# Performance work log

Hardware: AMD Instinct MI355X
Metric: run time of the kernel (lower is better)

Reference implementation:

```python
import jax, jax.numpy as jnp
import numpy as np

N_NODES = 50000
N_EDGES = 800000
HIDDEN = 128
NUM_GDL = 2


def setup_inputs() -> dict:
    key = jax.random.key(0)
    k0, k1, k2, k3, k4 = jax.random.split(key, 5)
    x = jax.random.normal(k0, (N_NODES, HIDDEN), dtype=jnp.float32)
    row = jax.random.randint(k1, (N_EDGES,), 0, N_NODES, dtype=jnp.int32)
    # ensure every node appears at least once as a target so degree >= 1
    col_tail = jax.random.randint(k2, (N_EDGES - N_NODES,), 0, N_NODES, dtype=jnp.int32)
    col = jnp.concatenate([jnp.arange(N_NODES, dtype=jnp.int32), col_tail])
    edge_index = jnp.stack([row, col], axis=0)  # [2, E]
    W1s = jax.random.normal(k3, (NUM_GDL, HIDDEN, HIDDEN), dtype=jnp.float32) / np.sqrt(HIDDEN).astype(np.float32)
    W2s = jax.random.normal(k4, (NUM_GDL, HIDDEN, 2 * HIDDEN), dtype=jnp.float32) / np.sqrt(2 * HIDDEN).astype(np.float32)
    biases = jnp.zeros((NUM_GDL, HIDDEN), dtype=jnp.float32)  # reset_parameters zeroes bias
    return {"x": x, "edge_index": edge_index, "W1s": W1s, "W2s": W2s, "biases": biases}


def reference(x, edge_index, W1s, W2s, biases):
    # eval mode: dropout is identity
    row, col = edge_index[0], edge_index[1]  # row = source j, col = target i
    n, d = x.shape
    deg = jax.ops.segment_sum(jnp.ones(row.shape[0], x.dtype), col, num_segments=n)
    norm = (1.0 / deg)[row]  # per-edge norm, indexed by row as in torch source
    for k in range(W1s.shape[0]):
        W1, W2, b = W1s[k], W2s[k], biases[k]
        # lin2(cat[x_i, x_j]) = x_i @ W2[:, :d].T + x_j @ W2[:, d:].T
        # precompute both node-level projections, then gather per edge (cheaper than per-edge GEMM)
        proj_i = x @ W2[:, :d].T  # [n, d]
        proj_j = x @ W2[:, d:].T  # [n, d]
        msg = norm[:, None] * (proj_i[col] + proj_j[row])  # [E, d]
        agg = jax.ops.segment_sum(msg, col, num_segments=n)  # scatter-add into targets
        out = x @ W1.T - agg + b
        x = jax.nn.gelu(out, approximate=False)  # torch nn.GELU default = exact erf
    return x
```

## Files before the change

kernel.cpp:

```cpp
#include <hip/hip_runtime.h>

#define N_NODES 50000
#define N_EDGES 800000
#define D 128
#define NBUCKET 196
#define CAP 8192
#define EPT 16
#define SCAT_BLOCKS 196
#define WCONV_BLOCKS 96
#define GEMM_TILES 782

typedef unsigned short ushort_t;
typedef __bf16 bf16x8 __attribute__((ext_vector_type(8)));
typedef float f32x4 __attribute__((ext_vector_type(4)));
typedef float f32x2 __attribute__((ext_vector_type(2)));

__device__ __forceinline__ ushort_t f2bf(float f) {
    unsigned u = __builtin_bit_cast(unsigned, f);
    u += 0x7FFFu + ((u >> 16) & 1u);
    return (ushort_t)(u >> 16);
}
__device__ __forceinline__ float bf2f(unsigned h16) {
    return __builtin_bit_cast(float, h16 << 16);
}
__device__ __forceinline__ bf16x8 pack8(float4 p0, float4 p1) {
    ushort_t __attribute__((aligned(16))) t[8] =
        { f2bf(p0.x), f2bf(p0.y), f2bf(p0.z), f2bf(p0.w),
          f2bf(p1.x), f2bf(p1.y), f2bf(p1.z), f2bf(p1.w) };
    return __builtin_bit_cast(bf16x8, *(const uint4*)t);
}

__global__ __launch_bounds__(256) void k_pre(const int* __restrict__ row, const int* __restrict__ col,
                                             int* __restrict__ bucket_cursor, unsigned* __restrict__ temp,
                                             const float* __restrict__ W1s, const float* __restrict__ W2s,
                                             ushort_t* __restrict__ Wb) {
    __shared__ int hist[NBUCKET];
    int b = blockIdx.x;
    if (b < SCAT_BLOCKS) {
        for (int t = threadIdx.x; t < NBUCKET; t += 256) hist[t] = 0;
        __syncthreads();
        int base = (b * 256 + threadIdx.x) * EPT;
        bool act = base < N_EDGES;
        int4 c[4], r[4];
        if (act) {
            #pragma unroll
            for (int q = 0; q < 4; ++q) c[q] = *(const int4*)(col + base + q * 4);
            #pragma unroll
            for (int q = 0; q < 4; ++q) r[q] = *(const int4*)(row + base + q * 4);
            #pragma unroll
            for (int q = 0; q < 4; ++q) {
                atomicAdd(&hist[c[q].x >> 8], 1); atomicAdd(&hist[c[q].y >> 8], 1);
                atomicAdd(&hist[c[q].z >> 8], 1); atomicAdd(&hist[c[q].w >> 8], 1);
            }
        }
        __syncthreads();
        for (int t = threadIdx.x; t < NBUCKET; t += 256) {
            int cnt = hist[t];
            hist[t] = cnt ? atomicAdd(&bucket_cursor[t], cnt) : 0;
        }
        __syncthreads();
        if (act) {
            #pragma unroll
            for (int q = 0; q < 4; ++q) {
                int cc[4] = { c[q].x, c[q].y, c[q].z, c[q].w };
                int rr[4] = { r[q].x, r[q].y, r[q].z, r[q].w };
                #pragma unroll
                for (int e = 0; e < 4; ++e) {
                    int bk = cc[e] >> 8;
                    int pos = atomicAdd(&hist[bk], 1);
                    temp[bk * CAP + pos] = (unsigned)rr[e] | ((unsigned)(cc[e] & 255) << 16);
                }
            }
        }
    } else {
        int c = (b - SCAT_BLOCKS) * 256 + threadIdx.x;
        int k = c / 12288, rem = c % 12288;
        int mat = rem / 4096, rr = (rem % 4096) / 32, col4 = rem % 32;
        const float* src = (mat == 0)
            ? (W1s + k * 16384 + rr * 128 + col4 * 4)
            : (W2s + k * 32768 + rr * 256 + (mat == 2 ? 128 : 0) + col4 * 4);
        float4 v = *(const float4*)src;
        ushort_t tmp[4] = { f2bf(v.x), f2bf(v.y), f2bf(v.z), f2bf(v.w) };
        *(uint2*)(Wb + ((size_t)(k * 3 + mat)) * 16384 + rr * 128 + col4 * 4) = *(const uint2*)tmp;
    }
}

template<bool AF32>
__device__ __forceinline__ void gemm_tile3(int m0, ushort_t (*Bs)[136],
                                           const void* __restrict__ xsrc,
                                           const ushort_t* __restrict__ Wl,
                                           const float* __restrict__ scl,
                                           ushort_t* __restrict__ Plb,
                                           ushort_t* __restrict__ Pi_,
                                           unsigned char* __restrict__ Pj8) {
    const int tid = threadIdx.x;
    const int w = tid >> 6, lane = tid & 63, quad = lane >> 4, r16 = lane & 15;
    const int gm = m0 + w * 16 + r16;
    bf16x8 a[4];
    if constexpr (AF32) {
        const float* xf = (const float*)xsrc;
        #pragma unroll
        for (int kk = 0; kk < 4; ++kk) {
            int colc = kk * 32 + quad * 8;
            float4 p0 = {0.f,0.f,0.f,0.f}, p1 = {0.f,0.f,0.f,0.f};
            if (gm < N_NODES) {
                p0 = *(const float4*)(xf + (size_t)gm * D + colc);
                p1 = *(const float4*)(xf + (size_t)gm * D + colc + 4);
            }
            a[kk] = pack8(p0, p1);
        }
    } else {
        const ushort_t* xb = (const ushort_t*)xsrc;
        #pragma unroll
        for (int kk = 0; kk < 4; ++kk) {
            int colc = kk * 32 + quad * 8;
            uint4 v0 = make_uint4(0,0,0,0);
            if (gm < N_NODES) v0 = *(const uint4*)(xb + (size_t)gm * D + colc);
            a[kk] = __builtin_bit_cast(bf16x8, v0);
        }
    }
    #pragma unroll
    for (int y = 0; y < 3; ++y) {
        const ushort_t* Wmat = Wl + (size_t)y * 16384;
        #pragma unroll
        for (int it = 0; it < 8; ++it) {
            int c = tid + it * 256;
            int r = c >> 4, kc = c & 15;
            *(uint4*)&Bs[r][kc * 8] = *(const uint4*)(Wmat + r * 128 + kc * 8);
        }
        __syncthreads();
        f32x4 acc[8];
        #pragma unroll
        for (int nt = 0; nt < 8; ++nt) acc[nt] = (f32x4){0.f, 0.f, 0.f, 0.f};
        #pragma unroll
        for (int kk = 0; kk < 4; ++kk) {
            #pragma unroll
            for (int nt = 0; nt < 8; ++nt) {
                bf16x8 b = __builtin_bit_cast(bf16x8,
                    *(const uint4*)&Bs[nt * 16 + r16][kk * 32 + quad * 8]);
                acc[nt] = __builtin_amdgcn_mfma_f32_16x16x32_bf16(b, a[kk], acc[nt], 0, 0, 0);
            }
        }
        if (gm < N_NODES) {
            if (y < 2) {
                ushort_t* Outp = (y == 0) ? Plb : Pi_;
                #pragma unroll
                for (int nt = 0; nt < 8; ++nt) {
                    ushort_t tmp[4] = { f2bf(acc[nt][0]), f2bf(acc[nt][1]),
                                        f2bf(acc[nt][2]), f2bf(acc[nt][3]) };
                    *(uint2*)(Outp + (size_t)gm * D + nt * 16 + quad * 4) = *(const uint2*)tmp;
                }
            } else {
                float sc = scl ? scl[gm] : 1.0f;
                #pragma unroll
                for (int nt = 0; nt < 8; ++nt) {
                    int v = __builtin_amdgcn_cvt_pk_fp8_f32(acc[nt][0] * sc, acc[nt][1] * sc, 0, false);
                    v = __builtin_amdgcn_cvt_pk_fp8_f32(acc[nt][2] * sc, acc[nt][3] * sc, v, true);
                    *(unsigned*)(Pj8 + (size_t)gm * D + nt * 16 + quad * 4) = (unsigned)v;
                }
            }
        }
        if (y < 2) __syncthreads();
    }
}

union __align__(16) LdsBG {
    ushort_t Bs[128][136];
    struct { int hist[256]; int sm[256]; } s;
};

__global__ __launch_bounds__(256) void k_bsort_gemm(const unsigned* __restrict__ temp,
                                                    const int* __restrict__ bucket_cursor,
                                                    ushort_t* __restrict__ csr, int* __restrict__ off,
                                                    int* __restrict__ deg, float* __restrict__ inv_deg,
                                                    const float* __restrict__ xf,
                                                    const ushort_t* __restrict__ Wb,
                                                    ushort_t* __restrict__ Plb,
                                                    ushort_t* __restrict__ Pi_,
                                                    unsigned char* __restrict__ Pj8) {
    __shared__ LdsBG lds;
    if (blockIdx.x < NBUCKET) {
        int* hist = lds.s.hist;
        int* sm = lds.s.sm;
        int b = blockIdx.x, t = threadIdx.x;
        int cnt = bucket_cursor[b];
        sm[t] = (t < b) ? bucket_cursor[t] : 0;
        __syncthreads();
        for (int o = 1; o < 256; o <<= 1) {
            int add = (t >= o) ? sm[t - o] : 0;
            __syncthreads();
            sm[t] += add;
            __syncthreads();
        }
        int gbase = sm[255];
        int tbase = b * CAP;
        hist[t] = 0;
        __syncthreads();
        int i = t;
        for (; i + 768 < cnt; i += 1024) {
            unsigned e0 = temp[tbase + i], e1 = temp[tbase + i + 256];
            unsigned e2 = temp[tbase + i + 512], e3 = temp[tbase + i + 768];
            atomicAdd(&hist[e0 >> 16], 1); atomicAdd(&hist[e1 >> 16], 1);
            atomicAdd(&hist[e2 >> 16], 1); atomicAdd(&hist[e3 >> 16], 1);
        }
        for (; i < cnt; i += 256) atomicAdd(&hist[temp[tbase + i] >> 16], 1);
        __syncthreads();
        int c = hist[t];
        sm[t] = c;
        __syncthreads();
        for (int o = 1; o < 256; o <<= 1) {
            int add = (t >= o) ? sm[t - o] : 0;
            __syncthreads();
            sm[t] += add;
            __syncthreads();
        }
        int excl = sm[t] - c;
        int node = b * 256 + t;
        if (node < N_NODES) {
            off[node] = gbase + excl;
            deg[node] = c;
            inv_deg[node] = 1.0f / (float)c;
        }
        __syncthreads();
        hist[t] = gbase + excl;
        __syncthreads();
        i = t;
        for (; i + 768 < cnt; i += 1024) {
            unsigned e0 = temp[tbase + i], e1 = temp[tbase + i + 256];
            unsigned e2 = temp[tbase + i + 512], e3 = temp[tbase + i + 768];
            int p0 = atomicAdd(&hist[e0 >> 16], 1);
            int p1 = atomicAdd(&hist[e1 >> 16], 1);
            int p2 = atomicAdd(&hist[e2 >> 16], 1);
            int p3 = atomicAdd(&hist[e3 >> 16], 1);
            csr[p0] = (ushort_t)e0; csr[p1] = (ushort_t)e1;
            csr[p2] = (ushort_t)e2; csr[p3] = (ushort_t)e3;
        }
        for (; i < cnt; i += 256) {
            unsigned e = temp[tbase + i];
            int p = atomicAdd(&hist[e >> 16], 1);
            csr[p] = (ushort_t)e;
        }
    } else {
        gemm_tile3<true>((blockIdx.x - NBUCKET) * 64, lds.Bs, xf, Wb, nullptr, Plb, Pi_, Pj8);
    }
}

__global__ __launch_bounds__(256) void k_gemm(const ushort_t* __restrict__ xb,
                                              const ushort_t* __restrict__ Wl,
                                              const float* __restrict__ inv_deg,
                                              ushort_t* __restrict__ Plb,
                                              ushort_t* __restrict__ Pi_,
                                              unsigned char* __restrict__ Pj8) {
    __shared__ __align__(16) ushort_t Bs[128][136];
    gemm_tile3<false>(blockIdx.x * 64, Bs, xb, Wl, inv_deg, Plb, Pi_, Pj8);
}

template<int LAYER0>
__device__ __forceinline__ void agg_body(const ushort_t* __restrict__ Plb,
                                         const ushort_t* __restrict__ Pi_,
                                         const unsigned char* __restrict__ Pj8,
                                         const int* __restrict__ off,
                                         const int* __restrict__ deg,
                                         const ushort_t* __restrict__ csr,
                                         const float* __restrict__ inv_deg,
                                         const float* __restrict__ bias,
                                         float* __restrict__ s_arr,
                                         float* __restrict__ out_f32,
                                         ushort_t* __restrict__ out_bf16) {
    int wv = __builtin_amdgcn_readfirstlane(threadIdx.x >> 6);
    int node = blockIdx.x * 4 + wv;
    if (node >= N_NODES) return;
    const int lane = threadIdx.x & 63;
    const int g = lane >> 4;
    const int q8 = lane & 15;
    const int eoff = 8 * q8 + 2 * g;
    unsigned ulin = *(const unsigned*)(Plb + (size_t)node * D + eoff);
    unsigned upi  = *(const unsigned*)(Pi_ + (size_t)node * D + eoff);
    float2 bv = *(const float2*)(bias + eoff);
    float su[8];
    #pragma unroll
    for (int k = 0; k < 8; ++k) su[k] = 0.f;
    float sd = 0.f;
    const int e0 = off[node], ne = deg[node];
    for (int j = 0; j < ne; j += 32) {
        int sx[8];
        float wt[8];
        #pragma unroll
        for (int t = 0; t < 8; ++t) {
            int idx = j + 4 * t + g;
            bool a = idx < ne;
            sx[t] = csr[e0 + (a ? idx : ne - 1)];
            wt[t] = a ? 1.f : 0.f;
        }
        uint2 uu[8];
        #pragma unroll
        for (int t = 0; t < 8; ++t) uu[t] = *(const uint2*)(Pj8 + (size_t)sx[t] * D + 8 * q8);
        float dv[8];
        if (LAYER0) {
            #pragma unroll
            for (int t = 0; t < 8; ++t) dv[t] = inv_deg[sx[t]] * wt[t];
        } else {
            #pragma unroll
            for (int t = 0; t < 8; ++t) dv[t] = wt[t];
        }
        #pragma unroll
        for (int t = 0; t < 8; ++t) {
            f32x2 f0 = __builtin_amdgcn_cvt_pk_f32_fp8((int)uu[t].x, false);
            f32x2 f1 = __builtin_amdgcn_cvt_pk_f32_fp8((int)uu[t].x, true);
            f32x2 f2 = __builtin_amdgcn_cvt_pk_f32_fp8((int)uu[t].y, false);
            f32x2 f3 = __builtin_amdgcn_cvt_pk_f32_fp8((int)uu[t].y, true);
            if (LAYER0) sd += dv[t];
            su[0] += dv[t] * f0[0]; su[1] += dv[t] * f0[1];
            su[2] += dv[t] * f1[0]; su[3] += dv[t] * f1[1];
            su[4] += dv[t] * f2[0]; su[5] += dv[t] * f2[1];
            su[6] += dv[t] * f3[0]; su[7] += dv[t] * f3[1];
        }
    }
    #pragma unroll
    for (int k = 0; k < 8; ++k) {
        su[k] += __shfl_xor(su[k], 16);
        su[k] += __shfl_xor(su[k], 32);
    }
    float si;
    if (LAYER0) {
        sd += __shfl_xor(sd, 16);
        sd += __shfl_xor(sd, 32);
        si = sd;
        if (lane == 0) s_arr[node] = si;
    } else {
        si = s_arr[node];
    }
    float t0 = (g < 2) ? ((g == 0) ? su[0] : su[2]) : ((g == 2) ? su[4] : su[6]);
    float t1 = (g < 2) ? ((g == 0) ? su[1] : su[3]) : ((g == 2) ? su[5] : su[7]);
    float a0 = bf2f(ulin & 0xffffu) + bv.x - si * bf2f(upi & 0xffffu) - t0;
    float a1 = bf2f(ulin >> 16)     + bv.y - si * bf2f(upi >> 16)     - t1;
    float g0 = 0.5f * a0 * (1.0f + erff(a0 * 0.70710678118654752440f));
    float g1 = 0.5f * a1 * (1.0f + erff(a1 * 0.70710678118654752440f));
    if (LAYER0) {
        ushort_t tmp[2] = { f2bf(g0), f2bf(g1) };
        *(unsigned*)(out_bf16 + (size_t)node * D + eoff) = *(const unsigned*)tmp;
    } else {
        *(float2*)(out_f32 + (size_t)node * D + eoff) = make_float2(g0, g1);
    }
}

__global__ __launch_bounds__(256) void k_agg0(const ushort_t* __restrict__ Plb,
                                              const ushort_t* __restrict__ Pi_,
                                              const unsigned char* __restrict__ Pj8,
                                              const int* __restrict__ off,
                                              const int* __restrict__ deg,
                                              const ushort_t* __restrict__ csr,
                                              const float* __restrict__ inv_deg,
                                              const float* __restrict__ bias,
                                              float* __restrict__ s_arr,
                                              ushort_t* __restrict__ out_bf16) {
    agg_body<1>(Plb, Pi_, Pj8, off, deg, csr, inv_deg, bias, s_arr, nullptr, out_bf16);
}

__global__ __launch_bounds__(256) void k_agg1(const ushort_t* __restrict__ Plb,
                                              const ushort_t* __restrict__ Pi_,
                                              const unsigned char* __restrict__ Pj8,
                                              const int* __restrict__ off,
                                              const int* __restrict__ deg,
                                              const ushort_t* __restrict__ csr,
                                              const float* __restrict__ inv_deg,
                                              const float* __restrict__ bias,
                                              float* __restrict__ s_arr,
                                              float* __restrict__ out_f32) {
    agg_body<0>(Plb, Pi_, Pj8, off, deg, csr, inv_deg, bias, s_arr, out_f32, nullptr);
}

extern "C" void kernel_launch(void* const* d_in, const int* in_sizes, int n_in,
                              void* d_out, int out_size, void* d_ws, size_t ws_size,
                              hipStream_t stream) {
    const float* x      = (const float*)d_in[0];
    const int*   ei     = (const int*)d_in[1];
    const int*   rowp   = ei;
    const int*   colp   = ei + N_EDGES;
    const float* W1s    = (const float*)d_in[2];
    const float* W2s    = (const float*)d_in[3];
    const float* biases = (const float*)d_in[4];
    float* out = (float*)d_out;

    char* ws = (char*)d_ws;
    size_t o = 0;
    auto carve = [&](size_t bytes) -> void* {
        void* p = ws + o;
        o = (o + bytes + 255) & ~(size_t)255;
        return p;
    };
    int*           bucket_cursor = (int*)carve(NBUCKET * 4);
    int*           deg     = (int*)carve(N_NODES * 4);
    float*         inv_deg = (float*)carve(N_NODES * 4);
    int*           off     = (int*)carve(N_NODES * 4);
    float*         s_arr   = (float*)carve(N_NODES * 4);
    ushort_t*      csr     = (ushort_t*)carve((size_t)N_EDGES * 2);
    unsigned*      temp    = (unsigned*)carve((size_t)NBUCKET * CAP * 4);
    ushort_t*      xb      = (ushort_t*)carve((size_t)N_NODES * D * 2);
    ushort_t*      Wb      = (ushort_t*)carve((size_t)2 * 3 * 16384 * 2);
    ushort_t*      Plb     = (ushort_t*)carve((size_t)N_NODES * D * 2);
    ushort_t*      Pi_     = (ushort_t*)carve((size_t)N_NODES * D * 2);
    unsigned char* Pj8     = (unsigned char*)carve((size_t)N_NODES * D);
    if (o > ws_size) return;

    hipMemsetAsync(bucket_cursor, 0, NBUCKET * 4, stream);

    k_pre<<<SCAT_BLOCKS + WCONV_BLOCKS, 256, 0, stream>>>(rowp, colp, bucket_cursor, temp,
                                                          W1s, W2s, Wb);
    k_bsort_gemm<<<NBUCKET + GEMM_TILES, 256, 0, stream>>>(temp, bucket_cursor, csr, off,
                                                           deg, inv_deg, x, Wb, Plb, Pi_, Pj8);

    const int AB = (N_NODES + 3) / 4;
    k_agg0<<<AB, 256, 0, stream>>>(Plb, Pi_, Pj8, off, deg, csr, inv_deg, biases, s_arr, xb);
    k_gemm<<<GEMM_TILES, 256, 0, stream>>>(xb, Wb + (size_t)3 * 16384, inv_deg, Plb, Pi_, Pj8);
    k_agg1<<<AB, 256, 0, stream>>>(Plb, Pi_, Pj8, off, deg, csr, inv_deg, biases + 128, s_arr, out);
}
```

Baseline: 192.3 us.

## Split GEMM per weight matrix, fuse weight bf16 conversion, grid-stride aggregation

```diff
diff --git a/kernel.cpp b/kernel.cpp
--- a/kernel.cpp
+++ b/kernel.cpp
@@ -7,8 +7,10 @@
 #define CAP 8192
 #define EPT 16
 #define SCAT_BLOCKS 196
-#define WCONV_BLOCKS 96
 #define GEMM_TILES 782
+#define GEMM_BLOCKS (GEMM_TILES * 3)
+#define AGG_UNITS 12500
+#define AGG_BLOCKS 2048
 
 typedef unsigned short ushort_t;
 typedef __bf16 bf16x8 __attribute__((ext_vector_type(8)));
@@ -31,71 +33,68 @@
 }
 
 __global__ __launch_bounds__(256) void k_pre(const int* __restrict__ row, const int* __restrict__ col,
-                                             int* __restrict__ bucket_cursor, unsigned* __restrict__ temp,
-                                             const float* __restrict__ W1s, const float* __restrict__ W2s,
-                                             ushort_t* __restrict__ Wb) {
+                                             int* __restrict__ bucket_cursor, unsigned* __restrict__ temp) {
     __shared__ int hist[NBUCKET];
     int b = blockIdx.x;
-    if (b < SCAT_BLOCKS) {
-        for (int t = threadIdx.x; t < NBUCKET; t += 256) hist[t] = 0;
-        __syncthreads();
-        int base = (b * 256 + threadIdx.x) * EPT;
-        bool act = base < N_EDGES;
-        int4 c[4], r[4];
-        if (act) {
+    for (int t = threadIdx.x; t < NBUCKET; t += 256) hist[t] = 0;
+    __syncthreads();
+    int base = (b * 256 + threadIdx.x) * EPT;
+    bool act = base < N_EDGES;
+    int4 c[4], r[4];
+    if (act) {
+        #pragma unroll
+        for (int q = 0; q < 4; ++q) c[q] = *(const int4*)(col + base + q * 4);
+        #pragma unroll
+        for (int q = 0; q < 4; ++q) r[q] = *(const int4*)(row + base + q * 4);
+        #pragma unroll
+        for (int q = 0; q < 4; ++q) {
+            atomicAdd(&hist[c[q].x >> 8], 1); atomicAdd(&hist[c[q].y >> 8], 1);
+            atomicAdd(&hist[c[q].z >> 8], 1); atomicAdd(&hist[c[q].w >> 8], 1);
+        }
+    }
+    __syncthreads();
+    for (int t = threadIdx.x; t < NBUCKET; t += 256) {
+        int cnt = hist[t];
+        hist[t] = cnt ? atomicAdd(&bucket_cursor[t], cnt) : 0;
+    }
+    __syncthreads();
+    if (act) {
+        #pragma unroll
+        for (int q = 0; q < 4; ++q) {
+            int cc[4] = { c[q].x, c[q].y, c[q].z, c[q].w };
+            int rr[4] = { r[q].x, r[q].y, r[q].z, r[q].w };
             #pragma unroll
-            for (int q = 0; q < 4; ++q) c[q] = *(const int4*)(col + base + q * 4);
-            #pragma unroll
-            for (int q = 0; q < 4; ++q) r[q] = *(const int4*)(row + base + q * 4);
-            #pragma unroll
-            for (int q = 0; q < 4; ++q) {
-                atomicAdd(&hist[c[q].x >> 8], 1); atomicAdd(&hist[c[q].y >> 8], 1);
-                atomicAdd(&hist[c[q].z >> 8], 1); atomicAdd(&hist[c[q].w >> 8], 1);
+            for (int e = 0; e < 4; ++e) {
+                int bk = cc[e] >> 8;
+                int pos = atomicAdd(&hist[bk], 1);
+                temp[bk * CAP + pos] = (unsigned)rr[e] | ((unsigned)(cc[e] & 255) << 16);
             }
         }
-        __syncthreads();
-        for (int t = threadIdx.x; t < NBUCKET; t += 256) {
-            int cnt = hist[t];
-            hist[t] = cnt ? atomicAdd(&bucket_cursor[t], cnt) : 0;
-        }
-        __syncthreads();
-        if (act) {
-            #pragma unroll
-            for (int q = 0; q < 4; ++q) {
-                int cc[4] = { c[q].x, c[q].y, c[q].z, c[q].w };
-                int rr[4] = { r[q].x, r[q].y, r[q].z, r[q].w };
-                #pragma unroll
-                for (int e = 0; e < 4; ++e) {
-                    int bk = cc[e] >> 8;
-                    int pos = atomicAdd(&hist[bk], 1);
-                    temp[bk * CAP + pos] = (unsigned)rr[e] | ((unsigned)(cc[e] & 255) << 16);
-                }
-            }
-        }
-    } else {
-        int c = (b - SCAT_BLOCKS) * 256 + threadIdx.x;
-        int k = c / 12288, rem = c % 12288;
-        int mat = rem / 4096, rr = (rem % 4096) / 32, col4 = rem % 32;
-        const float* src = (mat == 0)
-            ? (W1s + k * 16384 + rr * 128 + col4 * 4)
-            : (W2s + k * 32768 + rr * 256 + (mat == 2 ? 128 : 0) + col4 * 4);
-        float4 v = *(const float4*)src;
-        ushort_t tmp[4] = { f2bf(v.x), f2bf(v.y), f2bf(v.z), f2bf(v.w) };
-        *(uint2*)(Wb + ((size_t)(k * 3 + mat)) * 16384 + rr * 128 + col4 * 4) = *(const uint2*)tmp;
     }
 }
 
 template<bool AF32>
-__device__ __forceinline__ void gemm_tile3(int m0, ushort_t (*Bs)[136],
-                                           const void* __restrict__ xsrc,
-                                           const ushort_t* __restrict__ Wl,
-                                           const float* __restrict__ scl,
-                                           ushort_t* __restrict__ Plb,
-                                           ushort_t* __restrict__ Pi_,
-                                           unsigned char* __restrict__ Pj8) {
+__device__ __forceinline__ void gemm_tile_mat(int tile, int mat, ushort_t (*Bs)[136],
+                                              const void* __restrict__ xsrc,
+                                              const float* __restrict__ W1f,
+                                              const float* __restrict__ W2f,
+                                              const float* __restrict__ scl,
+                                              ushort_t* __restrict__ Plb,
+                                              ushort_t* __restrict__ Pi_,
+                                              unsigned char* __restrict__ Pj8) {
     const int tid = threadIdx.x;
     const int w = tid >> 6, lane = tid & 63, quad = lane >> 4, r16 = lane & 15;
-    const int gm = m0 + w * 16 + r16;
+    const int gm = tile * 64 + w * 16 + r16;
+    #pragma unroll
+    for (int it = 0; it < 8; ++it) {
+        int c = tid + it * 256;
+        int r = c >> 4, kc = c & 15;
+        const float* src = (mat == 0) ? (W1f + r * 128 + kc * 8)
+                                      : (W2f + r * 256 + (mat == 2 ? 128 : 0) + kc * 8);
+        float4 p0 = *(const float4*)src;
+        float4 p1 = *(const float4*)(src + 4);
+        *(uint4*)&Bs[r][kc * 8] = __builtin_bit_cast(uint4, pack8(p0, p1));
+    }
     bf16x8 a[4];
     if constexpr (AF32) {
         const float* xf = (const float*)xsrc;
@@ -119,48 +118,37 @@
             a[kk] = __builtin_bit_cast(bf16x8, v0);
         }
     }
+    __syncthreads();
+    f32x4 acc[8];
     #pragma unroll
-    for (int y = 0; y < 3; ++y) {
-        const ushort_t* Wmat = Wl + (size_t)y * 16384;
-        #pragma unroll
-        for (int it = 0; it < 8; ++it) {
-            int c = tid + it * 256;
-            int r = c >> 4, kc = c & 15;
-            *(uint4*)&Bs[r][kc * 8] = *(const uint4*)(Wmat + r * 128 + kc * 8);
-        }
-        __syncthreads();
-        f32x4 acc[8];
-        #pragma unroll
-        for (int nt = 0; nt < 8; ++nt) acc[nt] = (f32x4){0.f, 0.f, 0.f, 0.f};
-        #pragma unroll
-        for (int kk = 0; kk < 4; ++kk) {
+    for (int nt = 0; nt < 8; ++nt) acc[nt] = (f32x4){0.f, 0.f, 0.f, 0.f};
+    #pragma unroll
+    for (int kk = 0; kk < 4; ++kk) {
+        #pragma unroll
+        for (int nt = 0; nt < 8; ++nt) {
+            bf16x8 b = __builtin_bit_cast(bf16x8,
+                *(const uint4*)&Bs[nt * 16 + r16][kk * 32 + quad * 8]);
+            acc[nt] = __builtin_amdgcn_mfma_f32_16x16x32_bf16(b, a[kk], acc[nt], 0, 0, 0);
+        }
+    }
+    if (gm < N_NODES) {
+        if (mat < 2) {
+            ushort_t* Outp = (mat == 0) ? Plb : Pi_;
             #pragma unroll
             for (int nt = 0; nt < 8; ++nt) {
-                bf16x8 b = __builtin_bit_cast(bf16x8,
-                    *(const uint4*)&Bs[nt * 16 + r16][kk * 32 + quad * 8]);
-                acc[nt] = __builtin_amdgcn_mfma_f32_16x16x32_bf16(b, a[kk], acc[nt], 0, 0, 0);
+                ushort_t tmp[4] = { f2bf(acc[nt][0]), f2bf(acc[nt][1]),
+                                    f2bf(acc[nt][2]), f2bf(acc[nt][3]) };
+                *(uint2*)(Outp + (size_t)gm * D + nt * 16 + quad * 4) = *(const uint2*)tmp;
             }
-        }
-        if (gm < N_NODES) {
-            if (y < 2) {
-                ushort_t* Outp = (y == 0) ? Plb : Pi_;
-                #pragma unroll
-                for (int nt = 0; nt < 8; ++nt) {
-                    ushort_t tmp[4] = { f2bf(acc[nt][0]), f2bf(acc[nt][1]),
-                                        f2bf(acc[nt][2]), f2bf(acc[nt][3]) };
-                    *(uint2*)(Outp + (size_t)gm * D + nt * 16 + quad * 4) = *(const uint2*)tmp;
-                }
-            } else {
-                float sc = scl ? scl[gm] : 1.0f;
-                #pragma unroll
-                for (int nt = 0; nt < 8; ++nt) {
-                    int v = __builtin_amdgcn_cvt_pk_fp8_f32(acc[nt][0] * sc, acc[nt][1] * sc, 0, false);
-                    v = __builtin_amdgcn_cvt_pk_fp8_f32(acc[nt][2] * sc, acc[nt][3] * sc, v, true);
-                    *(unsigned*)(Pj8 + (size_t)gm * D + nt * 16 + quad * 4) = (unsigned)v;
-                }
+        } else {
+            float sc = scl ? scl[gm] : 1.0f;
+            #pragma unroll
+            for (int nt = 0; nt < 8; ++nt) {
+                int v = __builtin_amdgcn_cvt_pk_fp8_f32(acc[nt][0] * sc, acc[nt][1] * sc, 0, false);
+                v = __builtin_amdgcn_cvt_pk_fp8_f32(acc[nt][2] * sc, acc[nt][3] * sc, v, true);
+                *(unsigned*)(Pj8 + (size_t)gm * D + nt * 16 + quad * 4) = (unsigned)v;
             }
         }
-        if (y < 2) __syncthreads();
     }
 }
 
@@ -174,7 +162,8 @@
                                                     ushort_t* __restrict__ csr, int* __restrict__ off,
                                                     int* __restrict__ deg, float* __restrict__ inv_deg,
                                                     const float* __restrict__ xf,
-                                                    const ushort_t* __restrict__ Wb,
+                                                    const float* __restrict__ W1s,
+                                                    const float* __restrict__ W2s,
                                                     ushort_t* __restrict__ Plb,
                                                     ushort_t* __restrict__ Pi_,
                                                     unsigned char* __restrict__ Pj8) {
@@ -241,22 +230,25 @@
             csr[p] = (ushort_t)e;
         }
     } else {
-        gemm_tile3<true>((blockIdx.x - NBUCKET) * 64, lds.Bs, xf, Wb, nullptr, Plb, Pi_, Pj8);
+        int gid = blockIdx.x - NBUCKET;
+        gemm_tile_mat<true>(gid / 3, gid % 3, lds.Bs, xf, W1s, W2s, nullptr, Plb, Pi_, Pj8);
     }
 }
 
 __global__ __launch_bounds__(256) void k_gemm(const ushort_t* __restrict__ xb,
-                                              const ushort_t* __restrict__ Wl,
+                                              const float* __restrict__ W1f,
+                                              const float* __restrict__ W2f,
                                               const float* __restrict__ inv_deg,
                                               ushort_t* __restrict__ Plb,
                                               ushort_t* __restrict__ Pi_,
                                               unsigned char* __restrict__ Pj8) {
     __shared__ __align__(16) ushort_t Bs[128][136];
-    gemm_tile3<false>(blockIdx.x * 64, Bs, xb, Wl, inv_deg, Plb, Pi_, Pj8);
+    gemm_tile_mat<false>(blockIdx.x / 3, blockIdx.x % 3, Bs, xb, W1f, W2f, inv_deg, Plb, Pi_, Pj8);
 }
 
 template<int LAYER0>
-__device__ __forceinline__ void agg_body(const ushort_t* __restrict__ Plb,
+__device__ __forceinline__ void agg_unit(int u,
+                                         const ushort_t* __restrict__ Plb,
                                          const ushort_t* __restrict__ Pi_,
                                          const unsigned char* __restrict__ Pj8,
                                          const int* __restrict__ off,
@@ -268,8 +260,7 @@
                                          float* __restrict__ out_f32,
                                          ushort_t* __restrict__ out_bf16) {
     int wv = __builtin_amdgcn_readfirstlane(threadIdx.x >> 6);
-    int node = blockIdx.x * 4 + wv;
-    if (node >= N_NODES) return;
+    int node = u * 4 + wv;
     const int lane = threadIdx.x & 63;
     const int g = lane >> 4;
     const int q8 = lane & 15;
@@ -354,7 +345,8 @@
                                               const float* __restrict__ bias,
                                               float* __restrict__ s_arr,
                                               ushort_t* __restrict__ out_bf16) {
-    agg_body<1>(Plb, Pi_, Pj8, off, deg, csr, inv_deg, bias, s_arr, nullptr, out_bf16);
+    for (int u = blockIdx.x; u < AGG_UNITS; u += AGG_BLOCKS)
+        agg_unit<1>(u, Plb, Pi_, Pj8, off, deg, csr, inv_deg, bias, s_arr, nullptr, out_bf16);
 }
 
 __global__ __launch_bounds__(256) void k_agg1(const ushort_t* __restrict__ Plb,
@@ -367,7 +359,8 @@
                                               const float* __restrict__ bias,
                                               float* __restrict__ s_arr,
                                               float* __restrict__ out_f32) {
-    agg_body<0>(Plb, Pi_, Pj8, off, deg, csr, inv_deg, bias, s_arr, out_f32, nullptr);
+    for (int u = blockIdx.x; u < AGG_UNITS; u += AGG_BLOCKS)
+        agg_unit<0>(u, Plb, Pi_, Pj8, off, deg, csr, inv_deg, bias, s_arr, out_f32, nullptr);
 }
 
 extern "C" void kernel_launch(void* const* d_in, const int* in_sizes, int n_in,
@@ -397,7 +390,6 @@
     ushort_t*      csr     = (ushort_t*)carve((size_t)N_EDGES * 2);
     unsigned*      temp    = (unsigned*)carve((size_t)NBUCKET * CAP * 4);
     ushort_t*      xb      = (ushort_t*)carve((size_t)N_NODES * D * 2);
-    ushort_t*      Wb      = (ushort_t*)carve((size_t)2 * 3 * 16384 * 2);
     ushort_t*      Plb     = (ushort_t*)carve((size_t)N_NODES * D * 2);
     ushort_t*      Pi_     = (ushort_t*)carve((size_t)N_NODES * D * 2);
     unsigned char* Pj8     = (unsigned char*)carve((size_t)N_NODES * D);
@@ -405,13 +397,15 @@
 
     hipMemsetAsync(bucket_cursor, 0, NBUCKET * 4, stream);
 
-    k_pre<<<SCAT_BLOCKS + WCONV_BLOCKS, 256, 0, stream>>>(rowp, colp, bucket_cursor, temp,
-                                                          W1s, W2s, Wb);
-    k_bsort_gemm<<<NBUCKET + GEMM_TILES, 256, 0, stream>>>(temp, bucket_cursor, csr, off,
-                                                           deg, inv_deg, x, Wb, Plb, Pi_, Pj8);
-
-    const int AB = (N_NODES + 3) / 4;
-    k_agg0<<<AB, 256, 0, stream>>>(Plb, Pi_, Pj8, off, deg, csr, inv_deg, biases, s_arr, xb);
-    k_gemm<<<GEMM_TILES, 256, 0, stream>>>(xb, Wb + (size_t)3 * 16384, inv_deg, Plb, Pi_, Pj8);
-    k_agg1<<<AB, 256, 0, stream>>>(Plb, Pi_, Pj8, off, deg, csr, inv_deg, biases + 128, s_arr, out);
-}
+    k_pre<<<SCAT_BLOCKS, 256, 0, stream>>>(rowp, colp, bucket_cursor, temp);
+    k_bsort_gemm<<<NBUCKET + GEMM_BLOCKS, 256, 0, stream>>>(temp, bucket_cursor, csr, off,
+                                                            deg, inv_deg, x, W1s, W2s,
+                                                            Plb, Pi_, Pj8);
+
+    k_agg0<<<AGG_BLOCKS, 256, 0, stream>>>(Plb, Pi_, Pj8, off, deg, csr, inv_deg, biases,
+                                           s_arr, xb);
+    k_gemm<<<GEMM_BLOCKS, 256, 0, stream>>>(xb, W1s + 16384, W2s + 32768, inv_deg,
+                                            Plb, Pi_, Pj8);
+    k_agg1<<<AGG_BLOCKS, 256, 0, stream>>>(Plb, Pi_, Pj8, off, deg, csr, inv_deg, biases + 128,
+                                           s_arr, out);
+}
```

New measurement: 207.6 us. +7.9%, slower.
